# Optimization experiments

Measured on AMD Instinct MI355X. Metric: run time of the kernel, lower is better.

The kernel has to match this reference:

```python
import jax, jax.numpy as jnp
import numpy as np

N_NODES = 50000
N_EDGES = 800000
C_IN = 128
SIZES = [128, 128]
N_GRAPHS = 512
OUT = 5
BN_EPS = 1e-5


def setup_inputs() -> dict:
    key = jax.random.key(0)
    ks = jax.random.split(key, 24)
    s = 0.02
    inp = {
        "x": jax.random.normal(ks[0], (N_NODES, C_IN), dtype=jnp.float32),
        "edge_index": jax.random.randint(ks[1], (2, N_EDGES), 0, N_NODES, dtype=jnp.int32),
        "edge_weights": jax.random.uniform(ks[2], (N_EDGES, 1), dtype=jnp.float32),
        "batch": jnp.sort(jax.random.randint(ks[3], (N_NODES,), 0, N_GRAPHS, dtype=jnp.int32)),
    }
    c_in = C_IN
    ki = 4
    for l, c_out in enumerate(SIZES):
        inp[f"We{l}"] = jax.random.normal(ks[ki], (c_in, 1), dtype=jnp.float32) * s; ki += 1
        inp[f"be{l}"] = jnp.zeros((c_in,), dtype=jnp.float32)
        inp[f"W1_{l}"] = jax.random.normal(ks[ki], (c_out, c_in), dtype=jnp.float32) * s; ki += 1
        inp[f"b1_{l}"] = jnp.zeros((c_out,), dtype=jnp.float32)
        inp[f"g{l}"] = jnp.ones((c_out,), dtype=jnp.float32)
        inp[f"bt{l}"] = jnp.zeros((c_out,), dtype=jnp.float32)
        inp[f"W2_{l}"] = jax.random.normal(ks[ki], (c_out, c_out), dtype=jnp.float32) * s; ki += 1
        inp[f"b2_{l}"] = jnp.zeros((c_out,), dtype=jnp.float32)
        c_in = c_out
    inp["lin_w"] = jax.random.normal(ks[ki], (OUT, c_in), dtype=jnp.float32) * s
    inp["lin_b"] = jnp.zeros((OUT,), dtype=jnp.float32)
    return inp


def _mlp(h, W1, b1, g, bt, W2, b2):
    # PyG MLP(num_layers=2): Linear -> BatchNorm(train) -> ReLU -> Linear
    h = h @ W1.T + b1
    mu = h.mean(axis=0)
    var = jnp.mean((h - mu) ** 2, axis=0)
    h = (h - mu) * jax.lax.rsqrt(var + BN_EPS) * g + bt
    h = jax.nn.relu(h)
    return h @ W2.T + b2


def _gine_conv(x, src, dst, edge_weights, We, be, W1, b1, g, bt, W2, b2):
    edge_emb = edge_weights @ We.T + be          # [E, C] lin(edge_attr), edge_dim=1
    msg = jax.nn.relu(x[src] + edge_emb)          # gather + add + relu
    aggr = jax.ops.segment_sum(msg, dst, num_segments=x.shape[0])  # scatter-add
    return _mlp(x + aggr, W1, b1, g, bt, W2, b2)  # (1+eps)*x + aggr, eps=0


def reference(x, edge_index, edge_weights, batch,
              We0, be0, W1_0, b1_0, g0, bt0, W2_0, b2_0,
              We1, be1, W1_1, b1_1, g1, bt1, W2_1, b2_1,
              lin_w, lin_b):
    src, dst = edge_index[0], edge_index[1]
    x = jax.nn.relu(_gine_conv(x, src, dst, edge_weights, We0, be0, W1_0, b1_0, g0, bt0, W2_0, b2_0))
    x = jax.nn.relu(_gine_conv(x, src, dst, edge_weights, We1, be1, W1_1, b1_1, g1, bt1, W2_1, b2_1))
    pooled = jax.ops.segment_max(x, batch, num_segments=N_GRAPHS)  # global_max_pool
    return pooled @ lin_w.T + lin_b
```

## Files before the change

### kernel.cpp

```cpp
#include <hip/hip_runtime.h>

#define N_NODES 50000
#define N_EDGES 800000
#define C 128
#define N_GRAPHS 512
#define OUTDIM 5
#define BN_EPS 1e-5f
#define NB_SCAN 196
#define N_STRIPES 3125
#define SCAT_SUB 100

typedef short bs8 __attribute__((ext_vector_type(8)));
typedef float f32x4 __attribute__((ext_vector_type(4)));
typedef unsigned short us8 __attribute__((ext_vector_type(8)));

__device__ __forceinline__ unsigned short f2b(float f) {
    unsigned u = __float_as_uint(f);
    u += 0x7fffu + ((u >> 16) & 1u);
    return (unsigned short)(u >> 16);
}
__device__ __forceinline__ float b2f(unsigned v) {
    return __uint_as_float(v << 16);
}
__device__ __forceinline__ unsigned short f2h(float f) {
    union { _Float16 h; unsigned short s; } cv;
    cv.h = (_Float16)f;
    return cv.s;
}
__device__ __forceinline__ float h2f(unsigned short s) {
    union { unsigned short s; _Float16 h; } cv;
    cv.s = s;
    return (float)cv.h;
}

__global__ __launch_bounds__(256) void conv_kernel(const float* __restrict__ in,
                                                   unsigned short* __restrict__ out, int n4)
{
    int i = blockIdx.x * 256 + threadIdx.x;
    if (i < n4) {
        float4 v = reinterpret_cast<const float4*>(in)[i];
        ushort4 o;
        o.x = f2b(v.x); o.y = f2b(v.y); o.z = f2b(v.z); o.w = f2b(v.w);
        reinterpret_cast<ushort4*>(out)[i] = o;
    }
}

__global__ __launch_bounds__(256) void convw_kernel(const float* __restrict__ w0,
                                                    const float* __restrict__ w1,
                                                    const float* __restrict__ w2,
                                                    const float* __restrict__ w3,
                                                    unsigned short* __restrict__ out)
{
    const float* src[4] = {w0, w1, w2, w3};
    int m = blockIdx.x >> 4;
    int i = (blockIdx.x & 15) * 256 + threadIdx.x;
    float4 v = reinterpret_cast<const float4*>(src[m])[i];
    ushort4 o;
    o.x = f2b(v.x); o.y = f2b(v.y); o.z = f2b(v.z); o.w = f2b(v.w);
    reinterpret_cast<ushort4*>(out + m * 16384)[i] = o;
}

__global__ __launch_bounds__(256) void hist_kernel(const int* __restrict__ ei,
                                                   int* __restrict__ deg)
{
    int e = blockIdx.x * 256 + threadIdx.x;
    atomicAdd(&deg[ei[N_EDGES + e]], 1);
}

__global__ __launch_bounds__(256) void scan1_kernel(const int* __restrict__ deg,
                                                    int* __restrict__ rowptr,
                                                    int* __restrict__ bsum)
{
    __shared__ int sh[256];
    int tid = threadIdx.x;
    int i = blockIdx.x * 256 + tid;
    int v = (i < N_NODES) ? deg[i] : 0;
    sh[tid] = v;
    __syncthreads();
    #pragma unroll
    for (int off = 1; off < 256; off <<= 1) {
        int t = (tid >= off) ? sh[tid - off] : 0;
        __syncthreads();
        sh[tid] += t;
        __syncthreads();
    }
    if (i < N_NODES) rowptr[i] = sh[tid] - v;
    if (tid == 255) bsum[blockIdx.x] = sh[255];
}

__global__ __launch_bounds__(256) void scan2_kernel(int* __restrict__ bsum)
{
    __shared__ int sh[256];
    int tid = threadIdx.x;
    int v = (tid < NB_SCAN) ? bsum[tid] : 0;
    sh[tid] = v;
    __syncthreads();
    #pragma unroll
    for (int off = 1; off < 256; off <<= 1) {
        int t = (tid >= off) ? sh[tid - off] : 0;
        __syncthreads();
        sh[tid] += t;
        __syncthreads();
    }
    if (tid < NB_SCAN) bsum[tid] = sh[tid] - v;
}

__global__ __launch_bounds__(256) void scan3_kernel(const int* __restrict__ bsum,
                                                    int* __restrict__ rowptr,
                                                    int* __restrict__ cursor)
{
    int i = blockIdx.x * 256 + threadIdx.x;
    if (i < N_NODES) {
        int v = rowptr[i] + bsum[blockIdx.x];
        rowptr[i] = v;
        cursor[i] = v;
    }
    if (i == 0) rowptr[N_NODES] = N_EDGES;
}

__global__ __launch_bounds__(256) void scatter_kernel(const int* __restrict__ ei,
                                                      const float* __restrict__ ew,
                                                      int* __restrict__ cursor,
                                                      unsigned* __restrict__ csr)
{
    const int r   = blockIdx.x & 7;
    const int sub = blockIdx.x >> 3;
    const int lo  = r * (N_NODES / 8);
    const int hi  = lo + (N_NODES / 8);
    for (int e = sub * 256 + threadIdx.x; e < N_EDGES; e += SCAT_SUB * 256) {
        int dst = ei[N_EDGES + e];
        if (dst >= lo && dst < hi) {
            int pos = atomicAdd(&cursor[dst], 1);
            csr[pos] = ((unsigned)ei[e] << 16) | (unsigned)f2h(ew[e]);
        }
    }
}

__global__ __launch_bounds__(256) void aggr_kernel(const unsigned short* __restrict__ x,
                                                   const unsigned* __restrict__ csr,
                                                   const int* __restrict__ rowptr,
                                                   const float* __restrict__ We,
                                                   const float* __restrict__ be,
                                                   unsigned short* __restrict__ hout)
{
    int node = blockIdx.x * 4 + (threadIdx.x >> 6);
    int lane = threadIdx.x & 63;
    int c = lane * 2;
    float2 wev = *reinterpret_cast<const float2*>(&We[c]);
    float2 bev = *reinterpret_cast<const float2*>(&be[c]);
    int p = rowptr[node], p1 = rowptr[node + 1];
    unsigned sv = *reinterpret_cast<const unsigned*>(&x[(size_t)node * C + c]);
    float ax = b2f(sv & 0xffffu), ay = b2f(sv >> 16);
    for (; p + 4 <= p1; p += 4) {
        unsigned e0 = csr[p], e1 = csr[p + 1], e2 = csr[p + 2], e3 = csr[p + 3];
        float w0 = h2f((unsigned short)e0), w1 = h2f((unsigned short)e1);
        float w2 = h2f((unsigned short)e2), w3 = h2f((unsigned short)e3);
        unsigned g0 = *reinterpret_cast<const unsigned*>(&x[(size_t)(e0 >> 16) * C + c]);
        unsigned g1 = *reinterpret_cast<const unsigned*>(&x[(size_t)(e1 >> 16) * C + c]);
        unsigned g2 = *reinterpret_cast<const unsigned*>(&x[(size_t)(e2 >> 16) * C + c]);
        unsigned g3 = *reinterpret_cast<const unsigned*>(&x[(size_t)(e3 >> 16) * C + c]);
        float m;
        m = b2f(g0 & 0xffffu) + w0 * wev.x + bev.x; ax += fmaxf(m, 0.f);
        m = b2f(g0 >> 16)     + w0 * wev.y + bev.y; ay += fmaxf(m, 0.f);
        m = b2f(g1 & 0xffffu) + w1 * wev.x + bev.x; ax += fmaxf(m, 0.f);
        m = b2f(g1 >> 16)     + w1 * wev.y + bev.y; ay += fmaxf(m, 0.f);
        m = b2f(g2 & 0xffffu) + w2 * wev.x + bev.x; ax += fmaxf(m, 0.f);
        m = b2f(g2 >> 16)     + w2 * wev.y + bev.y; ay += fmaxf(m, 0.f);
        m = b2f(g3 & 0xffffu) + w3 * wev.x + bev.x; ax += fmaxf(m, 0.f);
        m = b2f(g3 >> 16)     + w3 * wev.y + bev.y; ay += fmaxf(m, 0.f);
    }
    for (; p < p1; ++p) {
        unsigned e0 = csr[p];
        float w0 = h2f((unsigned short)e0);
        unsigned g0 = *reinterpret_cast<const unsigned*>(&x[(size_t)(e0 >> 16) * C + c]);
        float m;
        m = b2f(g0 & 0xffffu) + w0 * wev.x + bev.x; ax += fmaxf(m, 0.f);
        m = b2f(g0 >> 16)     + w0 * wev.y + bev.y; ay += fmaxf(m, 0.f);
    }
    unsigned o = (unsigned)f2b(ax) | ((unsigned)f2b(ay) << 16);
    *reinterpret_cast<unsigned*>(&hout[(size_t)node * C + c]) = o;
}

template<int MODE>
__global__ __launch_bounds__(256) void mgemm_kernel(
    const unsigned short* __restrict__ A,
    const unsigned short* __restrict__ Wb,
    const float* __restrict__ bias,
    const float* __restrict__ scale,
    const float* __restrict__ shift,
    const int* __restrict__ batch,
    unsigned short* __restrict__ outb,
    float* __restrict__ pooled,
    float* __restrict__ gsum,
    float* __restrict__ gsq)
{
    __shared__ __align__(16) unsigned short xpose[4][16][40];
    const int wave = threadIdx.x >> 6;
    const int lane = threadIdx.x & 63;
    const int colbase = wave << 5;
    const int lr = lane & 15;
    const int lk = (lane >> 4) << 3;

    bs8 bf[2][4];
    #pragma unroll
    for (int ct = 0; ct < 2; ++ct)
        #pragma unroll
        for (int kc = 0; kc < 4; ++kc)
            bf[ct][kc] = *reinterpret_cast<const bs8*>(
                &Wb[(size_t)(colbase + ct * 16 + lr) * C + kc * 32 + lk]);

    const float bi0 = bias[colbase + lr];
    const float bi1 = bias[colbase + 16 + lr];

    float sc[4][8], sh[4][8];
    if (MODE >= 1) {
        #pragma unroll
        for (int kc = 0; kc < 4; ++kc)
            #pragma unroll
            for (int i = 0; i < 8; ++i) {
                sc[kc][i] = scale[kc * 32 + lk + i];
                sh[kc][i] = shift[kc * 32 + lk + i];
            }
    }

    float ssum0 = 0.f, ssq0 = 0.f, ssum1 = 0.f, ssq1 = 0.f;

    int s = blockIdx.x;
    bs8 raw[4];
    #pragma unroll
    for (int kc = 0; kc < 4; ++kc)
        raw[kc] = *reinterpret_cast<const bs8*>(
            &A[(size_t)(s * 16 + lr) * C + kc * 32 + lk]);

    while (true) {
        const int snext = s + gridDim.x;
        bs8 rawn[4];
        if (snext < N_STRIPES) {
            #pragma unroll
            for (int kc = 0; kc < 4; ++kc)
                rawn[kc] = *reinterpret_cast<const bs8*>(
                    &A[(size_t)(snext * 16 + lr) * C + kc * 32 + lk]);
        }

        bs8 af[4];
        #pragma unroll
        for (int kc = 0; kc < 4; ++kc) {
            if (MODE == 0) {
                af[kc] = raw[kc];
            } else {
                union { bs8 v; unsigned short u[8]; } pk;
                #pragma unroll
                for (int i = 0; i < 8; ++i) {
                    float f = b2f((unsigned)(unsigned short)raw[kc][i]);
                    pk.u[i] = f2b(fmaxf(f * sc[kc][i] + sh[kc][i], 0.f));
                }
                af[kc] = pk.v;
            }
        }

        f32x4 a0 = {0.f, 0.f, 0.f, 0.f};
        f32x4 a1 = {0.f, 0.f, 0.f, 0.f};
        #pragma unroll
        for (int kc = 0; kc < 4; ++kc) {
            a0 = __builtin_amdgcn_mfma_f32_16x16x32_bf16(af[kc], bf[0][kc], a0, 0, 0, 0);
            a1 = __builtin_amdgcn_mfma_f32_16x16x32_bf16(af[kc], bf[1][kc], a1, 0, 0, 0);
        }

        const int row0 = s << 4;
        if (MODE == 2) {
            const int orow = row0 + ((lane >> 4) << 2);
            float o0[4], o1[4];
            #pragma unroll
            for (int r = 0; r < 4; ++r) {
                o0[r] = fmaxf(a0[r] + bi0, 0.f);
                o1[r] = fmaxf(a1[r] + bi1, 0.f);
            }
            int gA = batch[orow], gB = batch[orow + 3];
            if (gA == gB) {
                float m0 = fmaxf(fmaxf(o0[0], o0[1]), fmaxf(o0[2], o0[3]));
                float m1 = fmaxf(fmaxf(o1[0], o1[1]), fmaxf(o1[2], o1[3]));
                atomicMax(reinterpret_cast<int*>(&pooled[(size_t)gA * C + colbase + lr]),
                          __float_as_int(m0));
                atomicMax(reinterpret_cast<int*>(&pooled[(size_t)gA * C + colbase + 16 + lr]),
                          __float_as_int(m1));
            } else {
                #pragma unroll
                for (int r = 0; r < 4; ++r) {
                    int g = batch[orow + r];
                    atomicMax(reinterpret_cast<int*>(&pooled[(size_t)g * C + colbase + lr]),
                              __float_as_int(o0[r]));
                    atomicMax(reinterpret_cast<int*>(&pooled[(size_t)g * C + colbase + 16 + lr]),
                              __float_as_int(o1[r]));
                }
            }
        } else {
            #pragma unroll
            for (int r = 0; r < 4; ++r) {
                int rl = ((lane >> 4) << 2) + r;
                float o0 = a0[r] + bi0;
                float o1 = a1[r] + bi1;
                if (MODE == 0) {
                    ssum0 += o0; ssq0 += o0 * o0;
                    ssum1 += o1; ssq1 += o1 * o1;
                } else {
                    o0 = fmaxf(o0, 0.f); o1 = fmaxf(o1, 0.f);
                }
                xpose[wave][rl][lr]      = f2b(o0);
                xpose[wave][rl][lr + 16] = f2b(o1);
            }
            __builtin_amdgcn_sched_barrier(0);
            us8 v = *reinterpret_cast<const us8*>(&xpose[wave][lane >> 2][(lane & 3) * 8]);
            *reinterpret_cast<us8*>(
                &outb[(size_t)(row0 + (lane >> 2)) * C + colbase + (lane & 3) * 8]) = v;
            __builtin_amdgcn_sched_barrier(0);
        }

        if (snext >= N_STRIPES) break;
        #pragma unroll
        for (int kc = 0; kc < 4; ++kc) raw[kc] = rawn[kc];
        s = snext;
    }

    if (MODE == 0) {
        ssum0 += __shfl_xor(ssum0, 16); ssum0 += __shfl_xor(ssum0, 32);
        ssq0  += __shfl_xor(ssq0, 16);  ssq0  += __shfl_xor(ssq0, 32);
        ssum1 += __shfl_xor(ssum1, 16); ssum1 += __shfl_xor(ssum1, 32);
        ssq1  += __shfl_xor(ssq1, 16);  ssq1  += __shfl_xor(ssq1, 32);
        if (lane < 16) {
            unsafeAtomicAdd(&gsum[colbase + lr], ssum0);
            unsafeAtomicAdd(&gsq[colbase + lr], ssq0);
            unsafeAtomicAdd(&gsum[colbase + 16 + lr], ssum1);
            unsafeAtomicAdd(&gsq[colbase + 16 + lr], ssq1);
        }
    }
}

__global__ void bnfin_kernel(const float* __restrict__ gsum, const float* __restrict__ gsq,
                             const float* __restrict__ g, const float* __restrict__ bt,
                             float* __restrict__ scale, float* __restrict__ shift)
{
    int c = threadIdx.x;
    float mu  = gsum[c] * (1.f / N_NODES);
    float var = gsq[c] * (1.f / N_NODES) - mu * mu;
    float rs  = rsqrtf(var + BN_EPS);
    float s   = rs * g[c];
    scale[c] = s;
    shift[c] = bt[c] - mu * s;
}

__global__ __launch_bounds__(64) void final_kernel(const float* __restrict__ pooled,
                                                   const float* __restrict__ lw,
                                                   const float* __restrict__ lb,
                                                   float* __restrict__ out)
{
    int gph = blockIdx.x;
    int lane = threadIdx.x;
    float v0 = pooled[(size_t)gph * C + lane];
    float v1 = pooled[(size_t)gph * C + lane + 64];
    for (int o = 0; o < OUTDIM; ++o) {
        float p = v0 * lw[o * C + lane] + v1 * lw[o * C + lane + 64];
        #pragma unroll
        for (int off = 32; off > 0; off >>= 1) p += __shfl_down(p, off);
        if (lane == 0) out[gph * OUTDIM + o] = p + lb[o];
    }
}

extern "C" void kernel_launch(void* const* d_in, const int* in_sizes, int n_in,
                              void* d_out, int out_size, void* d_ws, size_t ws_size,
                              hipStream_t stream)
{
    const float* x0   = (const float*)d_in[0];
    const int*   ei   = (const int*)  d_in[1];
    const float* ew   = (const float*)d_in[2];
    const int*   batch= (const int*)  d_in[3];
    const float* We0  = (const float*)d_in[4];
    const float* be0  = (const float*)d_in[5];
    const float* W1_0 = (const float*)d_in[6];
    const float* b1_0 = (const float*)d_in[7];
    const float* g0   = (const float*)d_in[8];
    const float* bt0  = (const float*)d_in[9];
    const float* W2_0 = (const float*)d_in[10];
    const float* b2_0 = (const float*)d_in[11];
    const float* We1  = (const float*)d_in[12];
    const float* be1  = (const float*)d_in[13];
    const float* W1_1 = (const float*)d_in[14];
    const float* b1_1 = (const float*)d_in[15];
    const float* g1   = (const float*)d_in[16];
    const float* bt1  = (const float*)d_in[17];
    const float* W2_1 = (const float*)d_in[18];
    const float* b2_1 = (const float*)d_in[19];
    const float* lin_w= (const float*)d_in[20];
    const float* lin_b= (const float*)d_in[21];

    char* base = (char*)d_ws;
    unsigned short* xb = (unsigned short*)(base);
    unsigned short* hA = (unsigned short*)(base + 12800000);
    unsigned short* tB = (unsigned short*)(base + 25600000);
    unsigned short* xC = (unsigned short*)(base + 38400000);
    unsigned short* Wb = (unsigned short*)(base + 51200000);
    unsigned* csr  = (unsigned*)(base + 51400000);
    int*    deg    = (int*)(base + 57800000);
    int*    rowptr = (int*)(base + 58000000);
    int*    cursor = (int*)(base + 58200008);
    int*    bsum   = (int*)(base + 58400008);
    float*  gsum   = (float*)(base + 58401024);
    float*  gsq    = gsum + 128;
    float*  scale  = gsq + 128;
    float*  shift  = scale + 128;
    float*  pooled = (float*)(base + 58403072);

    conv_kernel<<<6250, 256, 0, stream>>>(x0, xb, N_NODES * C / 4);
    convw_kernel<<<64, 256, 0, stream>>>(W1_0, W2_0, W1_1, W2_1, Wb);

    hipMemsetAsync(deg, 0, N_NODES * sizeof(int), stream);
    hist_kernel<<<N_EDGES / 256, 256, 0, stream>>>(ei, deg);
    scan1_kernel<<<NB_SCAN, 256, 0, stream>>>(deg, rowptr, bsum);
    scan2_kernel<<<1, 256, 0, stream>>>(bsum);
    scan3_kernel<<<NB_SCAN, 256, 0, stream>>>(bsum, rowptr, cursor);
    scatter_kernel<<<SCAT_SUB * 8, 256, 0, stream>>>(ei, ew, cursor, csr);

    aggr_kernel<<<N_NODES / 4, 256, 0, stream>>>(xb, csr, rowptr, We0, be0, hA);
    hipMemsetAsync(gsum, 0, 256 * sizeof(float), stream);
    mgemm_kernel<0><<<768, 256, 0, stream>>>(hA, Wb + 0 * 16384, b1_0,
                                             nullptr, nullptr, nullptr, tB, nullptr, gsum, gsq);
    bnfin_kernel<<<1, 128, 0, stream>>>(gsum, gsq, g0, bt0, scale, shift);
    mgemm_kernel<1><<<768, 256, 0, stream>>>(tB, Wb + 1 * 16384, b2_0,
                                             scale, shift, nullptr, xC, nullptr, nullptr, nullptr);

    aggr_kernel<<<N_NODES / 4, 256, 0, stream>>>(xC, csr, rowptr, We1, be1, hA);
    hipMemsetAsync(gsum, 0, 256 * sizeof(float), stream);
    mgemm_kernel<0><<<768, 256, 0, stream>>>(hA, Wb + 2 * 16384, b1_1,
                                             nullptr, nullptr, nullptr, tB, nullptr, gsum, gsq);
    bnfin_kernel<<<1, 128, 0, stream>>>(gsum, gsq, g1, bt1, scale, shift);
    hipMemsetAsync(pooled, 0, (size_t)N_GRAPHS * C * sizeof(float), stream);
    mgemm_kernel<2><<<768, 256, 0, stream>>>(tB, Wb + 3 * 16384, b2_1,
                                             scale, shift, batch, nullptr, pooled, nullptr, nullptr);

    final_kernel<<<N_GRAPHS, 64, 0, stream>>>(pooled, lin_w, lin_b, (float*)d_out);
}
```

Baseline: 384.6 us.

## Fuse edge aggregation into first MLP GEMM and fold BN finalize into second GEMM

Edge gather-aggregation now runs inside the first GEMM kernel. Each block aggregates 16 nodes into shared memory and then runs MFMA on them, so the hA intermediate is never written to or read back from global memory. The separate bnfin kernel is removed, and each mgemm block recomputes scale and shift from gsum and gsq itself. The cost is that aggregation now runs in only 768 persistent blocks with little latency hiding and no prefetch, where it used to have 12500 blocks. Four waves per block each do serial gather loops, which may hurt memory-level parallelism.

```diff
diff --git a/kernel.cpp b/kernel.cpp
--- a/kernel.cpp
+++ b/kernel.cpp
@@ -136,64 +136,19 @@
     }
 }
 
-__global__ __launch_bounds__(256) void aggr_kernel(const unsigned short* __restrict__ x,
-                                                   const unsigned* __restrict__ csr,
-                                                   const int* __restrict__ rowptr,
-                                                   const float* __restrict__ We,
-                                                   const float* __restrict__ be,
-                                                   unsigned short* __restrict__ hout)
-{
-    int node = blockIdx.x * 4 + (threadIdx.x >> 6);
-    int lane = threadIdx.x & 63;
-    int c = lane * 2;
-    float2 wev = *reinterpret_cast<const float2*>(&We[c]);
-    float2 bev = *reinterpret_cast<const float2*>(&be[c]);
-    int p = rowptr[node], p1 = rowptr[node + 1];
-    unsigned sv = *reinterpret_cast<const unsigned*>(&x[(size_t)node * C + c]);
-    float ax = b2f(sv & 0xffffu), ay = b2f(sv >> 16);
-    for (; p + 4 <= p1; p += 4) {
-        unsigned e0 = csr[p], e1 = csr[p + 1], e2 = csr[p + 2], e3 = csr[p + 3];
-        float w0 = h2f((unsigned short)e0), w1 = h2f((unsigned short)e1);
-        float w2 = h2f((unsigned short)e2), w3 = h2f((unsigned short)e3);
-        unsigned g0 = *reinterpret_cast<const unsigned*>(&x[(size_t)(e0 >> 16) * C + c]);
-        unsigned g1 = *reinterpret_cast<const unsigned*>(&x[(size_t)(e1 >> 16) * C + c]);
-        unsigned g2 = *reinterpret_cast<const unsigned*>(&x[(size_t)(e2 >> 16) * C + c]);
-        unsigned g3 = *reinterpret_cast<const unsigned*>(&x[(size_t)(e3 >> 16) * C + c]);
-        float m;
-        m = b2f(g0 & 0xffffu) + w0 * wev.x + bev.x; ax += fmaxf(m, 0.f);
-        m = b2f(g0 >> 16)     + w0 * wev.y + bev.y; ay += fmaxf(m, 0.f);
-        m = b2f(g1 & 0xffffu) + w1 * wev.x + bev.x; ax += fmaxf(m, 0.f);
-        m = b2f(g1 >> 16)     + w1 * wev.y + bev.y; ay += fmaxf(m, 0.f);
-        m = b2f(g2 & 0xffffu) + w2 * wev.x + bev.x; ax += fmaxf(m, 0.f);
-        m = b2f(g2 >> 16)     + w2 * wev.y + bev.y; ay += fmaxf(m, 0.f);
-        m = b2f(g3 & 0xffffu) + w3 * wev.x + bev.x; ax += fmaxf(m, 0.f);
-        m = b2f(g3 >> 16)     + w3 * wev.y + bev.y; ay += fmaxf(m, 0.f);
-    }
-    for (; p < p1; ++p) {
-        unsigned e0 = csr[p];
-        float w0 = h2f((unsigned short)e0);
-        unsigned g0 = *reinterpret_cast<const unsigned*>(&x[(size_t)(e0 >> 16) * C + c]);
-        float m;
-        m = b2f(g0 & 0xffffu) + w0 * wev.x + bev.x; ax += fmaxf(m, 0.f);
-        m = b2f(g0 >> 16)     + w0 * wev.y + bev.y; ay += fmaxf(m, 0.f);
-    }
-    unsigned o = (unsigned)f2b(ax) | ((unsigned)f2b(ay) << 16);
-    *reinterpret_cast<unsigned*>(&hout[(size_t)node * C + c]) = o;
-}
-
-template<int MODE>
-__global__ __launch_bounds__(256) void mgemm_kernel(
-    const unsigned short* __restrict__ A,
+__global__ __launch_bounds__(256) void famg_kernel(
+    const unsigned short* __restrict__ x,
+    const unsigned* __restrict__ csr,
+    const int* __restrict__ rowptr,
+    const float* __restrict__ We,
+    const float* __restrict__ be,
     const unsigned short* __restrict__ Wb,
     const float* __restrict__ bias,
-    const float* __restrict__ scale,
-    const float* __restrict__ shift,
-    const int* __restrict__ batch,
     unsigned short* __restrict__ outb,
-    float* __restrict__ pooled,
     float* __restrict__ gsum,
     float* __restrict__ gsq)
 {
+    __shared__ __align__(16) unsigned short hs[16][136];
     __shared__ __align__(16) unsigned short xpose[4][16][40];
     const int wave = threadIdx.x >> 6;
     const int lane = threadIdx.x & 63;
@@ -208,22 +163,141 @@
         for (int kc = 0; kc < 4; ++kc)
             bf[ct][kc] = *reinterpret_cast<const bs8*>(
                 &Wb[(size_t)(colbase + ct * 16 + lr) * C + kc * 32 + lk]);
-
     const float bi0 = bias[colbase + lr];
     const float bi1 = bias[colbase + 16 + lr];
 
+    const int c = lane * 2;
+    const float2 wev = *reinterpret_cast<const float2*>(&We[c]);
+    const float2 bev = *reinterpret_cast<const float2*>(&be[c]);
+
+    float ssum0 = 0.f, ssq0 = 0.f, ssum1 = 0.f, ssq1 = 0.f;
+
+    for (int s = blockIdx.x; s < N_STRIPES; s += gridDim.x) {
+        const int row0 = s << 4;
+
+        #pragma unroll
+        for (int i = 0; i < 4; ++i) {
+            int node = row0 + wave * 4 + i;
+            int p = rowptr[node], p1 = rowptr[node + 1];
+            unsigned sv = *reinterpret_cast<const unsigned*>(&x[(size_t)node * C + c]);
+            float ax = b2f(sv & 0xffffu), ay = b2f(sv >> 16);
+            for (; p + 4 <= p1; p += 4) {
+                unsigned e0 = csr[p], e1 = csr[p + 1], e2 = csr[p + 2], e3 = csr[p + 3];
+                float w0 = h2f((unsigned short)e0), w1 = h2f((unsigned short)e1);
+                float w2 = h2f((unsigned short)e2), w3 = h2f((unsigned short)e3);
+                unsigned g0 = *reinterpret_cast<const unsigned*>(&x[(size_t)(e0 >> 16) * C + c]);
+                unsigned g1 = *reinterpret_cast<const unsigned*>(&x[(size_t)(e1 >> 16) * C + c]);
+                unsigned g2 = *reinterpret_cast<const unsigned*>(&x[(size_t)(e2 >> 16) * C + c]);
+                unsigned g3 = *reinterpret_cast<const unsigned*>(&x[(size_t)(e3 >> 16) * C + c]);
+                float m;
+                m = b2f(g0 & 0xffffu) + w0 * wev.x + bev.x; ax += fmaxf(m, 0.f);
+                m = b2f(g0 >> 16)     + w0 * wev.y + bev.y; ay += fmaxf(m, 0.f);
+                m = b2f(g1 & 0xffffu) + w1 * wev.x + bev.x; ax += fmaxf(m, 0.f);
+                m = b2f(g1 >> 16)     + w1 * wev.y + bev.y; ay += fmaxf(m, 0.f);
+                m = b2f(g2 & 0xffffu) + w2 * wev.x + bev.x; ax += fmaxf(m, 0.f);
+                m = b2f(g2 >> 16)     + w2 * wev.y + bev.y; ay += fmaxf(m, 0.f);
+                m = b2f(g3 & 0xffffu) + w3 * wev.x + bev.x; ax += fmaxf(m, 0.f);
+                m = b2f(g3 >> 16)     + w3 * wev.y + bev.y; ay += fmaxf(m, 0.f);
+            }
+            for (; p < p1; ++p) {
+                unsigned e0 = csr[p];
+                float w0 = h2f((unsigned short)e0);
+                unsigned g0 = *reinterpret_cast<const unsigned*>(&x[(size_t)(e0 >> 16) * C + c]);
+                float m;
+                m = b2f(g0 & 0xffffu) + w0 * wev.x + bev.x; ax += fmaxf(m, 0.f);
+                m = b2f(g0 >> 16)     + w0 * wev.y + bev.y; ay += fmaxf(m, 0.f);
+            }
+            unsigned o = (unsigned)f2b(ax) | ((unsigned)f2b(ay) << 16);
+            *reinterpret_cast<unsigned*>(&hs[wave * 4 + i][c]) = o;
+        }
+        __syncthreads();
+
+        bs8 af[4];
+        #pragma unroll
+        for (int kc = 0; kc < 4; ++kc)
+            af[kc] = *reinterpret_cast<const bs8*>(&hs[lr][kc * 32 + lk]);
+        __syncthreads();
+
+        f32x4 a0 = {0.f, 0.f, 0.f, 0.f};
+        f32x4 a1 = {0.f, 0.f, 0.f, 0.f};
+        #pragma unroll
+        for (int kc = 0; kc < 4; ++kc) {
+            a0 = __builtin_amdgcn_mfma_f32_16x16x32_bf16(af[kc], bf[0][kc], a0, 0, 0, 0);
+            a1 = __builtin_amdgcn_mfma_f32_16x16x32_bf16(af[kc], bf[1][kc], a1, 0, 0, 0);
+        }
+
+        #pragma unroll
+        for (int r = 0; r < 4; ++r) {
+            int rl = ((lane >> 4) << 2) + r;
+            float o0 = a0[r] + bi0;
+            float o1 = a1[r] + bi1;
+            ssum0 += o0; ssq0 += o0 * o0;
+            ssum1 += o1; ssq1 += o1 * o1;
+            xpose[wave][rl][lr]      = f2b(o0);
+            xpose[wave][rl][lr + 16] = f2b(o1);
+        }
+        __builtin_amdgcn_sched_barrier(0);
+        us8 v = *reinterpret_cast<const us8*>(&xpose[wave][lane >> 2][(lane & 3) * 8]);
+        *reinterpret_cast<us8*>(
+            &outb[(size_t)(row0 + (lane >> 2)) * C + colbase + (lane & 3) * 8]) = v;
+        __builtin_amdgcn_sched_barrier(0);
+    }
+
+    ssum0 += __shfl_xor(ssum0, 16); ssum0 += __shfl_xor(ssum0, 32);
+    ssq0  += __shfl_xor(ssq0, 16);  ssq0  += __shfl_xor(ssq0, 32);
+    ssum1 += __shfl_xor(ssum1, 16); ssum1 += __shfl_xor(ssum1, 32);
+    ssq1  += __shfl_xor(ssq1, 16);  ssq1  += __shfl_xor(ssq1, 32);
+    if (lane < 16) {
+        unsafeAtomicAdd(&gsum[colbase + lr], ssum0);
+        unsafeAtomicAdd(&gsq[colbase + lr], ssq0);
+        unsafeAtomicAdd(&gsum[colbase + 16 + lr], ssum1);
+        unsafeAtomicAdd(&gsq[colbase + 16 + lr], ssq1);
+    }
+}
+
+template<int MODE>
+__global__ __launch_bounds__(256) void mgemm_kernel(
+    const unsigned short* __restrict__ A,
+    const unsigned short* __restrict__ Wb,
+    const float* __restrict__ bias,
+    const float* __restrict__ gsum,
+    const float* __restrict__ gsq,
+    const float* __restrict__ g,
+    const float* __restrict__ bt,
+    const int* __restrict__ batch,
+    unsigned short* __restrict__ outb,
+    float* __restrict__ pooled)
+{
+    __shared__ __align__(16) unsigned short xpose[4][16][40];
+    const int wave = threadIdx.x >> 6;
+    const int lane = threadIdx.x & 63;
+    const int colbase = wave << 5;
+    const int lr = lane & 15;
+    const int lk = (lane >> 4) << 3;
+
+    bs8 bf[2][4];
+    #pragma unroll
+    for (int ct = 0; ct < 2; ++ct)
+        #pragma unroll
+        for (int kc = 0; kc < 4; ++kc)
+            bf[ct][kc] = *reinterpret_cast<const bs8*>(
+                &Wb[(size_t)(colbase + ct * 16 + lr) * C + kc * 32 + lk]);
+
+    const float bi0 = bias[colbase + lr];
+    const float bi1 = bias[colbase + 16 + lr];
+
     float sc[4][8], sh[4][8];
-    if (MODE >= 1) {
-        #pragma unroll
-        for (int kc = 0; kc < 4; ++kc)
-            #pragma unroll
-            for (int i = 0; i < 8; ++i) {
-                sc[kc][i] = scale[kc * 32 + lk + i];
-                sh[kc][i] = shift[kc * 32 + lk + i];
-            }
-    }
-
-    float ssum0 = 0.f, ssq0 = 0.f, ssum1 = 0.f, ssq1 = 0.f;
+    #pragma unroll
+    for (int kc = 0; kc < 4; ++kc)
+        #pragma unroll
+        for (int i = 0; i < 8; ++i) {
+            int cc = kc * 32 + lk + i;
+            float mu  = gsum[cc] * (1.f / N_NODES);
+            float var = gsq[cc] * (1.f / N_NODES) - mu * mu;
+            float scv = rsqrtf(var + BN_EPS) * g[cc];
+            sc[kc][i] = scv;
+            sh[kc][i] = bt[cc] - mu * scv;
+        }
 
     int s = blockIdx.x;
     bs8 raw[4];
@@ -245,17 +319,13 @@
         bs8 af[4];
         #pragma unroll
         for (int kc = 0; kc < 4; ++kc) {
-            if (MODE == 0) {
-                af[kc] = raw[kc];
-            } else {
-                union { bs8 v; unsigned short u[8]; } pk;
-                #pragma unroll
-                for (int i = 0; i < 8; ++i) {
-                    float f = b2f((unsigned)(unsigned short)raw[kc][i]);
-                    pk.u[i] = f2b(fmaxf(f * sc[kc][i] + sh[kc][i], 0.f));
-                }
-                af[kc] = pk.v;
-            }
+            union { bs8 v; unsigned short u[8]; } pk;
+            #pragma unroll
+            for (int i = 0; i < 8; ++i) {
+                float f = b2f((unsigned)(unsigned short)raw[kc][i]);
+                pk.u[i] = f2b(fmaxf(f * sc[kc][i] + sh[kc][i], 0.f));
+            }
+            af[kc] = pk.v;
         }
 
         f32x4 a0 = {0.f, 0.f, 0.f, 0.f};
@@ -286,10 +356,10 @@
             } else {
                 #pragma unroll
                 for (int r = 0; r < 4; ++r) {
-                    int g = batch[orow + r];
-                    atomicMax(reinterpret_cast<int*>(&pooled[(size_t)g * C + colbase + lr]),
+                    int gg = batch[orow + r];
+                    atomicMax(reinterpret_cast<int*>(&pooled[(size_t)gg * C + colbase + lr]),
                               __float_as_int(o0[r]));
-                    atomicMax(reinterpret_cast<int*>(&pooled[(size_t)g * C + colbase + 16 + lr]),
+                    atomicMax(reinterpret_cast<int*>(&pooled[(size_t)gg * C + colbase + 16 + lr]),
                               __float_as_int(o1[r]));
                 }
             }
@@ -297,14 +367,8 @@
             #pragma unroll
             for (int r = 0; r < 4; ++r) {
                 int rl = ((lane >> 4) << 2) + r;
-                float o0 = a0[r] + bi0;
-                float o1 = a1[r] + bi1;
-                if (MODE == 0) {
-                    ssum0 += o0; ssq0 += o0 * o0;
-                    ssum1 += o1; ssq1 += o1 * o1;
-                } else {
-                    o0 = fmaxf(o0, 0.f); o1 = fmaxf(o1, 0.f);
-                }
+                float o0 = fmaxf(a0[r] + bi0, 0.f);
+                float o1 = fmaxf(a1[r] + bi1, 0.f);
                 xpose[wave][rl][lr]      = f2b(o0);
                 xpose[wave][rl][lr + 16] = f2b(o1);
             }
@@ -320,32 +384,6 @@
         for (int kc = 0; kc < 4; ++kc) raw[kc] = rawn[kc];
         s = snext;
     }
-
-    if (MODE == 0) {
-        ssum0 += __shfl_xor(ssum0, 16); ssum0 += __shfl_xor(ssum0, 32);
-        ssq0  += __shfl_xor(ssq0, 16);  ssq0  += __shfl_xor(ssq0, 32);
-        ssum1 += __shfl_xor(ssum1, 16); ssum1 += __shfl_xor(ssum1, 32);
-        ssq1  += __shfl_xor(ssq1, 16);  ssq1  += __shfl_xor(ssq1, 32);
-        if (lane < 16) {
-            unsafeAtomicAdd(&gsum[colbase + lr], ssum0);
-            unsafeAtomicAdd(&gsq[colbase + lr], ssq0);
-            unsafeAtomicAdd(&gsum[colbase + 16 + lr], ssum1);
-            unsafeAtomicAdd(&gsq[colbase + 16 + lr], ssq1);
-        }
-    }
-}
-
-__global__ void bnfin_kernel(const float* __restrict__ gsum, const float* __restrict__ gsq,
-                             const float* __restrict__ g, const float* __restrict__ bt,
-                             float* __restrict__ scale, float* __restrict__ shift)
-{
-    int c = threadIdx.x;
-    float mu  = gsum[c] * (1.f / N_NODES);
-    float var = gsq[c] * (1.f / N_NODES) - mu * mu;
-    float rs  = rsqrtf(var + BN_EPS);
-    float s   = rs * g[c];
-    scale[c] = s;
-    shift[c] = bt[c] - mu * s;
 }
 
 __global__ __launch_bounds__(64) void final_kernel(const float* __restrict__ pooled,
@@ -394,7 +432,6 @@
 
     char* base = (char*)d_ws;
     unsigned short* xb = (unsigned short*)(base);
-    unsigned short* hA = (unsigned short*)(base + 12800000);
     unsigned short* tB = (unsigned short*)(base + 25600000);
     unsigned short* xC = (unsigned short*)(base + 38400000);
     unsigned short* Wb = (unsigned short*)(base + 51200000);
@@ -405,8 +442,6 @@
     int*    bsum   = (int*)(base + 58400008);
     float*  gsum   = (float*)(base + 58401024);
     float*  gsq    = gsum + 128;
-    float*  scale  = gsq + 128;
-    float*  shift  = scale + 128;
     float*  pooled = (float*)(base + 58403072);
 
     conv_kernel<<<6250, 256, 0, stream>>>(x0, xb, N_NODES * C / 4);
@@ -419,22 +454,18 @@
     scan3_kernel<<<NB_SCAN, 256, 0, stream>>>(bsum, rowptr, cursor);
     scatter_kernel<<<SCAT_SUB * 8, 256, 0, stream>>>(ei, ew, cursor, csr);
 
-    aggr_kernel<<<N_NODES / 4, 256, 0, stream>>>(xb, csr, rowptr, We0, be0, hA);
     hipMemsetAsync(gsum, 0, 256 * sizeof(float), stream);
-    mgemm_kernel<0><<<768, 256, 0, stream>>>(hA, Wb + 0 * 16384, b1_0,
-                                             nullptr, nullptr, nullptr, tB, nullptr, gsum, gsq);
-    bnfin_kernel<<<1, 128, 0, stream>>>(gsum, gsq, g0, bt0, scale, shift);
+    famg_kernel<<<768, 256, 0, stream>>>(xb, csr, rowptr, We0, be0,
+                                         Wb + 0 * 16384, b1_0, tB, gsum, gsq);
     mgemm_kernel<1><<<768, 256, 0, stream>>>(tB, Wb + 1 * 16384, b2_0,
-                                             scale, shift, nullptr, xC, nullptr, nullptr, nullptr);
-
-    aggr_kernel<<<N_NODES / 4, 256, 0, stream>>>(xC, csr, rowptr, We1, be1, hA);
+                                             gsum, gsq, g0, bt0, nullptr, xC, nullptr);
+
     hipMemsetAsync(gsum, 0, 256 * sizeof(float), stream);
-    mgemm_kernel<0><<<768, 256, 0, stream>>>(hA, Wb + 2 * 16384, b1_1,
-                                             nullptr, nullptr, nullptr, tB, nullptr, gsum, gsq);
-    bnfin_kernel<<<1, 128, 0, stream>>>(gsum, gsq, g1, bt1, scale, shift);
+    famg_kernel<<<768, 256, 0, stream>>>(xC, csr, rowptr, We1, be1,
+                                         Wb + 2 * 16384, b1_1, tB, gsum, gsq);
     hipMemsetAsync(pooled, 0, (size_t)N_GRAPHS * C * sizeof(float), stream);
     mgemm_kernel<2><<<768, 256, 0, stream>>>(tB, Wb + 3 * 16384, b2_1,
-                                             scale, shift, batch, nullptr, pooled, nullptr, nullptr);
+                                             gsum, gsq, g1, bt1, batch, nullptr, pooled);
 
     final_kernel<<<N_GRAPHS, 64, 0, stream>>>(pooled, lin_w, lin_b, (float*)d_out);
 }
```

New measurement: 430.4 us. 11.9% more time.
